# Kernel optimization log

Measured on AMD Instinct MI355X. Metric: run time of the kernel, lower is better.

Reference implementation:

```python
import jax, jax.numpy as jnp
import numpy as np

B, S, D, E, F = 2, 2048, 1024, 14, 2048


def setup_inputs() -> dict:
    key = jax.random.key(0)
    k = jax.random.split(key, 4)
    h = jax.random.normal(k[0], (B, S, D), dtype=jnp.float32)
    router_w = jax.random.normal(k[1], (D, E), dtype=jnp.float32) * 0.02
    # kaiming-uniform-like scale for expert weights
    w1 = jax.random.uniform(k[2], (E, D, F), dtype=jnp.float32,
                            minval=-1.0, maxval=1.0) * float(np.sqrt(6.0 / D))
    w2 = jax.random.uniform(k[3], (E, F, D), dtype=jnp.float32,
                            minval=-1.0, maxval=1.0) * float(np.sqrt(6.0 / F))
    b1 = jnp.zeros((E, F), dtype=jnp.float32)
    b2 = jnp.zeros((E, D), dtype=jnp.float32)
    return {"h": h, "router_w": router_w, "w1": w1, "b1": b1, "w2": w2, "b2": b2}


def reference(h, router_w, w1, b1, w2, b2):
    Bb, Ss, Dd = h.shape
    x = h.reshape(-1, Dd)                                  # (N, D)
    logits = x @ router_w                                  # (N, E)
    assignments = jnp.argmax(logits, axis=-1)              # (N,) phase B routing
    probs = jax.nn.softmax(logits, axis=-1)
    weights = jnp.take_along_axis(probs, assignments[:, None], axis=1)[:, 0]  # (N,)
    # dense all-expert FFN (as in the original module)
    hid = jnp.einsum('nd,edf->nef', x, w1) + b1            # (N, E, F)
    hid = jax.nn.gelu(hid, approximate=False)
    all_out = jnp.einsum('nef,efd->ned', hid, w2) + b2     # (N, E, D)
    sel = jnp.take_along_axis(all_out, assignments[:, None, None], axis=1)[:, 0, :]
    moe_out = (sel * weights[:, None]).reshape(Bb, Ss, Dd)
    return moe_out
```

## Files before the change

kernel.cpp:

```cpp
#include <hip/hip_runtime.h>
#include <hip/hip_bf16.h>


#define NTOK 4096
#define NEXP 14
#define DDIM 1024
#define FDIM 2048

typedef __attribute__((ext_vector_type(8))) short short8;
typedef __attribute__((ext_vector_type(4))) float floatx4;

__device__ __forceinline__ unsigned bfr(float f) {
  unsigned u = __float_as_uint(f);
  return (u + 0x7FFFu + ((u >> 16) & 1u)) >> 16;
}
__device__ __forceinline__ unsigned pk2(float a, float b) {
  return bfr(a) | (bfr(b) << 16);
}

__device__ __forceinline__ void gload16(const void* g, void* l) {
  __builtin_amdgcn_global_load_lds((const __attribute__((address_space(1))) void*)g,
                                   (__attribute__((address_space(3))) void*)l, 16, 0, 0);
}

struct GemmSh {
  char sA[2][16384];
  char sB[2][8192];
  int tokL[128];
  float wgtL[128];
};
union FuseSh {
  GemmSh g;
  float t32[4096];
};

__global__ void k_init(const float* __restrict__ rw, float* __restrict__ rwT) {
  int i = blockIdx.x * 256 + threadIdx.x;
  if (i < DDIM * NEXP) rwT[(i % NEXP) * DDIM + i / NEXP] = rw[i];
}

__device__ __forceinline__ void router_body(
    int bid, const float* __restrict__ x, const float* __restrict__ rwT,
    int* __restrict__ assign, float* __restrict__ wgt,
    unsigned short* __restrict__ h16) {
  int wid = threadIdx.x >> 6, lane = threadIdx.x & 63;
  int n = bid * 4 + wid;
  const float* xr = x + (size_t)n * DDIM;
  unsigned short* hr = h16 + (size_t)n * DDIM;
  double acc[NEXP];
#pragma unroll
  for (int e = 0; e < NEXP; e++) acc[e] = 0.0;
#pragma unroll
  for (int i = 0; i < 4; i++) {
    int d0 = i * 256 + lane * 4;
    float4 xv = *(const float4*)(xr + d0);
    uint2 hb;
    hb.x = pk2(xv.x, xv.y);
    hb.y = pk2(xv.z, xv.w);
    *(uint2*)(hr + d0) = hb;
    double x0 = xv.x, x1 = xv.y, x2 = xv.z, x3 = xv.w;
#pragma unroll
    for (int e = 0; e < NEXP; e++) {
      float4 rv = *(const float4*)(rwT + e * DDIM + d0);
      acc[e] += x0 * (double)rv.x + x1 * (double)rv.y + x2 * (double)rv.z + x3 * (double)rv.w;
    }
  }
#pragma unroll
  for (int e = 0; e < NEXP; e++)
    for (int m = 32; m > 0; m >>= 1) acc[e] += __shfl_xor(acc[e], m, 64);
  int best = 0;
  double bv = acc[0];
#pragma unroll
  for (int e = 1; e < NEXP; e++)
    if (acc[e] > bv) { bv = acc[e]; best = e; }
  float s = 0.f;
#pragma unroll
  for (int e = 0; e < NEXP; e++) s += expf((float)(acc[e] - bv));
  if (lane == 0) {
    wgt[n] = 1.0f / s;
    assign[n] = best;
  }
}

__device__ __forceinline__ void prep_body(float* __restrict__ t32,
                                          const float* __restrict__ W,
                                          unsigned short* __restrict__ img,
                                          int K, int N, int b) {
  int KB = K >> 6, NB = N >> 6, K4 = KB >> 2;
  int kb4 = b % K4;
  int nb_ = b / K4;
  int nblk = nb_ % NB, e = nb_ / NB;
  int t = threadIdx.x;
  int k = t >> 4, n4 = (t & 15) * 4;
  for (int z = 0; z < 4; z++) {
    int kblk = kb4 * 4 + z;
    const float* src = W + (size_t)e * K * N + (size_t)(kblk * 64) * N + nblk * 64;
#pragma unroll
    for (int j = 0; j < 4; j++) {
      int kk = k + j * 16;
      float4 v = *(const float4*)(src + (size_t)kk * N + n4);
      int sw = kk & 31;
      t32[kk * 64 + ((n4 + 0) ^ sw)] = v.x;
      t32[kk * 64 + ((n4 + 1) ^ sw)] = v.y;
      t32[kk * 64 + ((n4 + 2) ^ sw)] = v.z;
      t32[kk * 64 + ((n4 + 3) ^ sw)] = v.w;
    }
    __syncthreads();
    unsigned short* dst = img + (size_t)((e * NB + nblk) * KB + kblk) * 4096;
#pragma unroll
    for (int c = 0; c < 2; c++) {
      int ci = t + c * 256;
      int col = ci >> 3, q = ci & 7, k8 = q ^ (col & 7);
      float f[8];
#pragma unroll
      for (int j = 0; j < 8; j++) {
        int kk = k8 * 8 + j;
        f[j] = t32[kk * 64 + (col ^ (kk & 31))];
      }
      uint4 o;
      o.x = pk2(f[0], f[1]);
      o.y = pk2(f[2], f[3]);
      o.z = pk2(f[4], f[5]);
      o.w = pk2(f[6], f[7]);
      *(uint4*)(dst + ci * 8) = o;
    }
    __syncthreads();
  }
}

__global__ __launch_bounds__(256) void k_fuseA(
    const float* __restrict__ x, const float* __restrict__ rwT,
    int* __restrict__ assign, float* __restrict__ wgt,
    unsigned short* __restrict__ h16,
    const float* __restrict__ w1, unsigned short* __restrict__ img1) {
  __shared__ float t32[4096];
  int bid = blockIdx.x;
  if (bid < NTOK / 4) {
    router_body(bid, x, rwT, assign, wgt, h16);
  } else {
    prep_body(t32, w1, img1, DDIM, FDIM, bid - NTOK / 4);
  }
}

__global__ __launch_bounds__(1024) void k_sort(
    const int* __restrict__ assign, int* __restrict__ cnt,
    int* __restrict__ list, int* __restrict__ tiles, int* __restrict__ ntl) {
  __shared__ int clds[64][NEXP];
  __shared__ int tot[16];
  __shared__ int tstart[NEXP + 1];
  int tid = threadIdx.x;
  int wv = tid >> 6, lane = tid & 63;
  unsigned long long below = (1ull << lane) - 1ull;
  int e4[4], r4[4];
#pragma unroll
  for (int t = 0; t < 4; t++) {
    int n = wv * 256 + t * 64 + lane;
    int e = assign[n];
    int rank = 0, gcnt = 0;
#pragma unroll
    for (int xx = 0; xx < NEXP; xx++) {
      unsigned long long m = __ballot(e == xx);
      if (e == xx) rank = __popcll(m & below);
      if (lane == xx) gcnt = __popcll(m);
    }
    e4[t] = e;
    r4[t] = rank;
    if (lane < NEXP) clds[wv * 4 + t][lane] = gcnt;
  }
  __syncthreads();
  if (wv < NEXP) {
    int v = clds[lane][wv];
    int s = v;
    for (int m = 1; m < 64; m <<= 1) {
      int t = __shfl_up(s, m, 64);
      if (lane >= m) s += t;
    }
    clds[lane][wv] = s - v;
    if (lane == 63) {
      cnt[wv] = s;
      tot[wv] = s;
    }
  }
  __syncthreads();
#pragma unroll
  for (int t = 0; t < 4; t++) {
    int n = wv * 256 + t * 64 + lane;
    int e = e4[t];
    int pos = clds[wv * 4 + t][e] + r4[t];
    list[e * NTOK + pos] = n;
  }
  if (wv == 15) {
    int c = (lane < NEXP) ? tot[lane] : 0;
    int nt = (c + 127) >> 7;
    int st = nt;
    for (int m = 1; m < 64; m <<= 1) {
      int t = __shfl_up(st, m, 64);
      if (lane >= m) st += t;
    }
    if (lane < NEXP) tstart[lane] = st - nt;
    if (lane == NEXP - 1) {
      tstart[NEXP] = st;
      *ntl = st;
    }
    int totT = __shfl(st, NEXP - 1, 64);
    if (lane < totT) {
      int e = 0;
      while (tstart[e + 1] <= lane) e++;
      tiles[2 * lane] = e;
      tiles[2 * lane + 1] = (lane - tstart[e]) * 128;
    }
  }
}

template <int LAYER>
__device__ __forceinline__ void gemm_body(
    GemmSh* sh, int tI, int n0,
    const unsigned short* __restrict__ Xb, const unsigned short* __restrict__ img,
    const float* __restrict__ Bias, const float* __restrict__ wgt,
    unsigned short* __restrict__ outB, float* __restrict__ outF,
    const int* __restrict__ wsI, const int* __restrict__ list) {
  constexpr int K = (LAYER == 1) ? DDIM : FDIM;
  constexpr int N = (LAYER == 1) ? FDIM : DDIM;
  constexpr int NIT = K / 64;
  constexpr int KB = K / 64, NB = N / 64;

  const int* cnt = wsI;
  const int* ntl = wsI + 48;
  const int* tiles = wsI + 64;

  if (tI >= *ntl) return;
  int e = tiles[2 * tI], m0 = tiles[2 * tI + 1];
  int rows = cnt[e] - m0;
  int base = e * NTOK + m0;

  char (*sA)[16384] = sh->sA;
  char (*sB)[8192] = sh->sB;
  int* tokL = sh->tokL;
  float* wgtL = sh->wgtL;

  int tid = threadIdx.x;
  if (tid < 128) {
    int tok = list[base + tid] & (NTOK - 1);
    tokL[tid] = tok;
    if (LAYER == 2) wgtL[tid] = wgt[tok];
  }
  __syncthreads();

  int lane = tid & 63, wid = tid >> 6, wm = wid >> 1, wn = wid & 1;

  const char* gA[4];
  {
    unsigned sw = (unsigned)(((lane & 7) * 16) ^ ((lane >> 3) << 4));
#pragma unroll
    for (int j = 0; j < 4; j++) {
      int row = wid * 32 + j * 8 + (lane >> 3);
      gA[j] = (const char*)(Xb + (size_t)tokL[row] * K) + sw;
    }
  }
  const char* gB = (const char*)img +
                   (size_t)((e * NB + (n0 >> 6)) * KB) * 8192 + wid * 2048 + lane * 16;

  floatx4 acc[4][2];
#pragma unroll
  for (int i = 0; i < 4; i++)
#pragma unroll
    for (int j = 0; j < 2; j++) acc[i][j] = (floatx4){0.f, 0.f, 0.f, 0.f};

#define GLOAD_AB(it, p)                                                     \
  do {                                                                      \
    _Pragma("unroll") for (int j = 0; j < 4; j++)                           \
        gload16(gA[j] + (size_t)(it) * 128, sA[p] + (wid * 4 + j) * 1024);  \
    _Pragma("unroll") for (int j = 0; j < 2; j++)                           \
        gload16(gB + (size_t)(it) * 8192 + j * 1024,                        \
                sB[p] + wid * 2048 + j * 1024);                             \
  } while (0)

#define MFMA_PHASE(P)                                                                    \
  do {                                                                                   \
    const char* A_ = sA[P];                                                              \
    const char* B_ = sB[P];                                                              \
    _Pragma("unroll") for (int kc = 0; kc < 2; kc++) {                                   \
      short8 af[4], bf[2];                                                               \
      int kb = kc * 64 + ((lane >> 4) << 4);                                             \
      _Pragma("unroll") for (int f = 0; f < 4; f++) {                                    \
        int rr = wm * 64 + f * 16 + (lane & 15);                                         \
        af[f] = *(const short8*)(A_ + rr * 128 + (kb ^ ((rr & 7) << 4)));                \
      }                                                                                  \
      _Pragma("unroll") for (int f = 0; f < 2; f++) {                                    \
        int cc = wn * 32 + f * 16 + (lane & 15);                                         \
        bf[f] = *(const short8*)(B_ + cc * 128 + (kb ^ ((cc & 7) << 4)));                \
      }                                                                                  \
      _Pragma("unroll") for (int fm = 0; fm < 4; fm++)                                   \
      _Pragma("unroll") for (int fn = 0; fn < 2; fn++)                                   \
          acc[fm][fn] =                                                                  \
              __builtin_amdgcn_mfma_f32_16x16x32_bf16(af[fm], bf[fn], acc[fm][fn], 0, 0, 0); \
    }                                                                                    \
  } while (0)

  GLOAD_AB(0, 0);
  for (int it = 0; it < NIT - 1; ++it) {
    int p = it & 1;
    __builtin_amdgcn_sched_barrier(0);
    __builtin_amdgcn_s_barrier();
    GLOAD_AB(it + 1, p ^ 1);
    __builtin_amdgcn_sched_barrier(0);
    asm volatile("s_waitcnt vmcnt(6)" ::: "memory");
    __builtin_amdgcn_s_barrier();
    __builtin_amdgcn_sched_barrier(0);
    MFMA_PHASE(p);
  }
  {
    int p = (NIT - 1) & 1;
    __builtin_amdgcn_sched_barrier(0);
    __builtin_amdgcn_s_barrier();
    asm volatile("s_waitcnt vmcnt(0)" ::: "memory");
    __builtin_amdgcn_s_barrier();
    __builtin_amdgcn_sched_barrier(0);
    MFMA_PHASE(p);
  }
#undef GLOAD_AB
#undef MFMA_PHASE

  float bv[2];
#pragma unroll
  for (int f = 0; f < 2; f++) bv[f] = Bias[(size_t)e * N + n0 + wn * 32 + f * 16 + (lane & 15)];
#pragma unroll
  for (int fm = 0; fm < 4; fm++) {
#pragma unroll
    for (int r = 0; r < 4; r++) {
      int gr = wm * 64 + fm * 16 + ((lane >> 4) << 2) + r;
      if (gr < rows) {
        int tok = tokL[gr];
#pragma unroll
        for (int fn = 0; fn < 2; fn++) {
          int col = n0 + wn * 32 + fn * 16 + (lane & 15);
          float v = acc[fm][fn][r] + bv[fn];
          if (LAYER == 1) {
            v = 0.5f * v * (1.0f + erff(v * 0.70710678118654752f));
            outB[(size_t)tok * FDIM + col] = (unsigned short)bfr(v);
          } else {
            outF[(size_t)tok * DDIM + col] = v * wgtL[gr];
          }
        }
      }
    }
  }
}

__global__ __launch_bounds__(256, 3) void k_fuseB(
    const unsigned short* __restrict__ h16, const unsigned short* __restrict__ img1,
    const float* __restrict__ b1, unsigned short* __restrict__ hid,
    const int* __restrict__ wsI, const int* __restrict__ list,
    const float* __restrict__ w2, unsigned short* __restrict__ img2) {
  __shared__ FuseSh sh;
  int bid = blockIdx.x;
  if (bid < (FDIM / 64) * 45) {
    gemm_body<1>(&sh.g, bid >> 5, (bid & 31) << 6, h16, img1, b1, nullptr, hid,
                 nullptr, wsI, list);
  } else {
    prep_body(sh.t32, w2, img2, FDIM, DDIM, bid - (FDIM / 64) * 45);
  }
}

__global__ __launch_bounds__(256, 3) void k_gemm2(
    const unsigned short* __restrict__ hid, const unsigned short* __restrict__ img2,
    const float* __restrict__ b2, const float* __restrict__ wgt,
    float* __restrict__ outF, const int* __restrict__ wsI,
    const int* __restrict__ list) {
  __shared__ GemmSh sh;
  gemm_body<2>(&sh, blockIdx.y, blockIdx.x << 6, hid, img2, b2, wgt, nullptr,
               outF, wsI, list);
}

extern "C" void kernel_launch(void* const* d_in, const int* in_sizes, int n_in,
                              void* d_out, int out_size, void* d_ws, size_t ws_size,
                              hipStream_t stream) {
  const float* h  = (const float*)d_in[0];
  const float* rw = (const float*)d_in[1];
  const float* w1 = (const float*)d_in[2];
  const float* b1 = (const float*)d_in[3];
  const float* w2 = (const float*)d_in[4];
  const float* b2 = (const float*)d_in[5];
  float* out = (float*)d_out;

  int* wsI = (int*)d_ws;
  int* assign = wsI + 160;
  float* wgt = (float*)(wsI + 4256);
  int* list = (int*)((char*)d_ws + 65536);
  float* rwT = (float*)((char*)d_ws + 294912);
  unsigned short* hid  = (unsigned short*)((char*)d_ws + 393216);
  unsigned short* h16  = (unsigned short*)((char*)d_ws + 17170432);
  unsigned short* img1 = (unsigned short*)((char*)d_ws + 25559040);
  unsigned short* img2 = (unsigned short*)((char*)d_ws + 54919168);

  k_init<<<56, 256, 0, stream>>>(rw, rwT);
  k_fuseA<<<NTOK / 4 + 1792, 256, 0, stream>>>(h, rwT, assign, wgt, h16, w1, img1);
  k_sort<<<1, 1024, 0, stream>>>(assign, wsI, list, wsI + 64, wsI + 48);
  k_fuseB<<<1440 + 1792, 256, 0, stream>>>(h16, img1, b1, hid, wsI, list, w2, img2);
  k_gemm2<<<dim3(DDIM / 64, 45), 256, 0, stream>>>(hid, img2, b2, wgt, out, wsI, list);
}
```

Before: 166.6 us.

## Restructure weight prep into fewer blocks converting 128-wide column strips over full K

Weight conversion to the bf16 tiled image now runs each block over an entire K range for a 128-column strip, loading full 512-byte row segments instead of 256-byte ones. Prep blocks drop from 1792 to 224 for w1 and 112 for w2. The goal is wider, more coalesced global reads and less per-block overhead. In exchange, LDS staging per block doubles and each block runs much longer, so far fewer blocks remain to overlap with the router and GEMM1 blocks, which can leave a long tail.

```diff
diff --git a/kernel.cpp b/kernel.cpp
--- a/kernel.cpp
+++ b/kernel.cpp
@@ -31,7 +31,7 @@
 };
 union FuseSh {
   GemmSh g;
-  float t32[4096];
+  float t32[8192];
 };
 
 __global__ void k_init(const float* __restrict__ rw, float* __restrict__ rwT) {
@@ -82,47 +82,52 @@
   }
 }
 
-__device__ __forceinline__ void prep_body(float* __restrict__ t32,
-                                          const float* __restrict__ W,
-                                          unsigned short* __restrict__ img,
-                                          int K, int N, int b) {
-  int KB = K >> 6, NB = N >> 6, K4 = KB >> 2;
-  int kb4 = b % K4;
-  int nb_ = b / K4;
-  int nblk = nb_ % NB, e = nb_ / NB;
+__device__ __forceinline__ void prep_body2(float* __restrict__ t32,
+                                           const float* __restrict__ W,
+                                           unsigned short* __restrict__ img,
+                                           int K, int N, int b) {
+  int KB = K >> 6, NB = N >> 6, NB2 = N >> 7;
+  int nb2 = b % NB2, e = b / NB2;
   int t = threadIdx.x;
-  int k = t >> 4, n4 = (t & 15) * 4;
-  for (int z = 0; z < 4; z++) {
-    int kblk = kb4 * 4 + z;
-    const float* src = W + (size_t)e * K * N + (size_t)(kblk * 64) * N + nblk * 64;
-#pragma unroll
-    for (int j = 0; j < 4; j++) {
-      int kk = k + j * 16;
-      float4 v = *(const float4*)(src + (size_t)kk * N + n4);
-      int sw = kk & 31;
-      t32[kk * 64 + ((n4 + 0) ^ sw)] = v.x;
-      t32[kk * 64 + ((n4 + 1) ^ sw)] = v.y;
-      t32[kk * 64 + ((n4 + 2) ^ sw)] = v.z;
-      t32[kk * 64 + ((n4 + 3) ^ sw)] = v.w;
+  const float* base = W + (size_t)e * K * N + nb2 * 128;
+  for (int kblk = 0; kblk < KB; ++kblk) {
+    const float* src = base + (size_t)(kblk * 64) * N;
+#pragma unroll
+    for (int j = 0; j < 8; j++) {
+      int f = t + 256 * j;
+      int row = f >> 5, c4 = f & 31;
+      float4 v = *(const float4*)(src + (size_t)row * N + c4 * 4);
+      int sw = row & 31;
+#pragma unroll
+      for (int c = 0; c < 4; c++) {
+        int col = c4 * 4 + c;
+        int sub = col >> 6, n = col & 63;
+        float val = (c == 0) ? v.x : (c == 1) ? v.y : (c == 2) ? v.z : v.w;
+        t32[row * 128 + sub * 64 + (((n + sub) & 63) ^ sw)] = val;
+      }
     }
     __syncthreads();
-    unsigned short* dst = img + (size_t)((e * NB + nblk) * KB + kblk) * 4096;
-#pragma unroll
-    for (int c = 0; c < 2; c++) {
-      int ci = t + c * 256;
-      int col = ci >> 3, q = ci & 7, k8 = q ^ (col & 7);
-      float f[8];
-#pragma unroll
-      for (int j = 0; j < 8; j++) {
-        int kk = k8 * 8 + j;
-        f[j] = t32[kk * 64 + (col ^ (kk & 31))];
+#pragma unroll
+    for (int sub = 0; sub < 2; sub++) {
+      unsigned short* dst =
+          img + (size_t)((e * NB + nb2 * 2 + sub) * KB + kblk) * 4096;
+#pragma unroll
+      for (int c = 0; c < 2; c++) {
+        int ci = t + c * 256;
+        int col = ci >> 3, q = ci & 7, k8 = q ^ (col & 7);
+        float f[8];
+#pragma unroll
+        for (int j = 0; j < 8; j++) {
+          int kk = k8 * 8 + j;
+          f[j] = t32[kk * 128 + sub * 64 + (((col + sub) & 63) ^ (kk & 31))];
+        }
+        uint4 o;
+        o.x = pk2(f[0], f[1]);
+        o.y = pk2(f[2], f[3]);
+        o.z = pk2(f[4], f[5]);
+        o.w = pk2(f[6], f[7]);
+        *(uint4*)(dst + ci * 8) = o;
       }
-      uint4 o;
-      o.x = pk2(f[0], f[1]);
-      o.y = pk2(f[2], f[3]);
-      o.z = pk2(f[4], f[5]);
-      o.w = pk2(f[6], f[7]);
-      *(uint4*)(dst + ci * 8) = o;
     }
     __syncthreads();
   }
@@ -133,12 +138,12 @@
     int* __restrict__ assign, float* __restrict__ wgt,
     unsigned short* __restrict__ h16,
     const float* __restrict__ w1, unsigned short* __restrict__ img1) {
-  __shared__ float t32[4096];
+  __shared__ float t32[8192];
   int bid = blockIdx.x;
   if (bid < NTOK / 4) {
     router_body(bid, x, rwT, assign, wgt, h16);
   } else {
-    prep_body(t32, w1, img1, DDIM, FDIM, bid - NTOK / 4);
+    prep_body2(t32, w1, img1, DDIM, FDIM, bid - NTOK / 4);
   }
 }
 
@@ -358,7 +363,7 @@
     gemm_body<1>(&sh.g, bid >> 5, (bid & 31) << 6, h16, img1, b1, nullptr, hid,
                  nullptr, wsI, list);
   } else {
-    prep_body(sh.t32, w2, img2, FDIM, DDIM, bid - (FDIM / 64) * 45);
+    prep_body2(sh.t32, w2, img2, FDIM, DDIM, bid - (FDIM / 64) * 45);
   }
 }
 
@@ -394,8 +399,8 @@
   unsigned short* img2 = (unsigned short*)((char*)d_ws + 54919168);
 
   k_init<<<56, 256, 0, stream>>>(rw, rwT);
-  k_fuseA<<<NTOK / 4 + 1792, 256, 0, stream>>>(h, rwT, assign, wgt, h16, w1, img1);
+  k_fuseA<<<NTOK / 4 + 224, 256, 0, stream>>>(h, rwT, assign, wgt, h16, w1, img1);
   k_sort<<<1, 1024, 0, stream>>>(assign, wsI, list, wsI + 64, wsI + 48);
-  k_fuseB<<<1440 + 1792, 256, 0, stream>>>(h16, img1, b1, hid, wsI, list, w2, img2);
+  k_fuseB<<<1440 + 112, 256, 0, stream>>>(h16, img1, b1, hid, wsI, list, w2, img2);
   k_gemm2<<<dim3(DDIM / 64, 45), 256, 0, stream>>>(hid, img2, b2, wgt, out, wsI, list);
 }
```

New measurement: 262.7 us. 57.7% more time.
